# Performance work log

Hardware: AMD Instinct MI355X
Metric: run time of the kernel (lower is better)

## Reference

```python
import jax, jax.numpy as jnp
import numpy as np

NEG = -1e30  # finite stand-in for -inf (keeps grads nan-free)
BLANK = 0


def _ctc_nll(log_probs, targets, input_lengths, target_lengths):
    """Per-sample CTC negative log-likelihood.
    log_probs: (B,T,V) log-softmax outputs; targets: (B,S) int; lengths: (B,)."""
    B, T, V = log_probs.shape
    S = targets.shape[1]
    L = 2 * S + 1
    # extended label sequence: blank, y1, blank, y2, ..., blank -> (B, L)
    ext = jnp.full((B, L), BLANK, dtype=targets.dtype).at[:, 1::2].set(targets)
    # skip transition (l-2 -> l) allowed iff ext[l] != blank and ext[l] != ext[l-2]
    prev2 = jnp.pad(ext[:, :-2], ((0, 0), (2, 0)), constant_values=-1)
    skip = (ext != BLANK) & (ext != prev2)  # (B, L)

    def emit(lp_t):  # lp_t: (B,V) -> (B,L)
        return jnp.take_along_axis(lp_t, ext, axis=1)

    alpha0 = jnp.where(jnp.arange(L)[None, :] < 2, emit(log_probs[:, 0]), NEG)

    def step(alpha, lp_t):
        p1 = jnp.pad(alpha[:, :-1], ((0, 0), (1, 0)), constant_values=NEG)
        p2 = jnp.pad(alpha[:, :-2], ((0, 0), (2, 0)), constant_values=NEG)
        p2 = jnp.where(skip, p2, NEG)
        m = jnp.maximum(alpha, jnp.maximum(p1, p2))
        lse = m + jnp.log(jnp.exp(alpha - m) + jnp.exp(p1 - m) + jnp.exp(p2 - m))
        new = lse + emit(lp_t)
        return new, new

    # scan over time; collect alphas so we can read them at each sample's T_b-1
    _, alphas_rest = jax.lax.scan(step, alpha0, jnp.swapaxes(log_probs, 0, 1)[1:])
    alphas = jnp.concatenate([alpha0[None], alphas_rest], axis=0)  # (T,B,L)
    alphas = jnp.swapaxes(alphas, 0, 1)  # (B,T,L)
    alpha_T = jnp.take_along_axis(
        alphas, (input_lengths - 1)[:, None, None], axis=1)[:, 0]  # (B,L)

    end1 = jnp.take_along_axis(alpha_T, (2 * target_lengths)[:, None], axis=1)[:, 0]
    end2 = jnp.take_along_axis(alpha_T, (2 * target_lengths - 1)[:, None], axis=1)[:, 0]
    m = jnp.maximum(end1, end2)
    ll = m + jnp.log(jnp.exp(end1 - m) + jnp.exp(end2 - m))
    return -ll  # (B,)


def setup_inputs() -> dict:
    key = jax.random.key(0)
    k1, k2, k3, k4 = jax.random.split(key, 4)
    B, T, V, S = 32, 2000, 1024, 256
    log_probs = jax.nn.log_softmax(
        jax.random.normal(k1, (B, T, V), dtype=jnp.float32), axis=-1)
    targets = jax.random.randint(k2, (B, S), 1, V)  # exclude blank=0
    input_lengths = jax.random.randint(k3, (B,), 1500, T + 1)
    target_lengths = jax.random.randint(k4, (B,), 128, S + 1)
    return {"log_probs": log_probs, "targets": targets,
            "input_lengths": input_lengths, "target_lengths": target_lengths}


def reference(log_probs, targets, input_lengths, target_lengths):
    nll = _ctc_nll(log_probs, targets, input_lengths, target_lengths)
    # zero_infinity=True: drop infeasible samples
    nll = jnp.where(nll > 0.5 * (-NEG), 0.0, nll)
    # reduction='mean': divide each loss by its target length, then batch-mean
    return jnp.mean(nll / target_lengths.astype(nll.dtype))
```

## Files before the change

### kernel.cpp

```cpp
#include <hip/hip_runtime.h>
#include <stdint.h>


#define LN2F 0.69314718055994530942f
#define PD 16

__device__ __forceinline__ float shr1f(float x) {
  return __int_as_float(
      __builtin_amdgcn_update_dpp(0, __float_as_int(x), 0x138, 0xF, 0xF, true));
}
__device__ __forceinline__ int shr1i(int x) {
  return __builtin_amdgcn_update_dpp(0, x, 0x138, 0xF, 0xF, true);
}

__global__ __launch_bounds__(256) void k_gather_exp(
    const float* __restrict__ lp, const int* __restrict__ tgt,
    const int* __restrict__ ilen, float* __restrict__ El,
    float* __restrict__ Eb, int T, int V, int S) {
  const int b = blockIdx.y;
  const int t = blockIdx.x;
  if (t >= ilen[b]) return;
  const int tid = threadIdx.x;
  const int lab = tgt[b * S + tid];
  const float* row = lp + ((size_t)b * T + t) * V;
  El[((size_t)b * T + t) * S + tid] = __expf(row[lab]);
  if (tid == 0) Eb[(size_t)b * T + t] = __expf(row[0]);
}

__global__ __launch_bounds__(64) void k_ctc_alpha(
    const float* __restrict__ El, const float* __restrict__ Eb,
    const int* __restrict__ tgt, const int* __restrict__ ilen,
    const int* __restrict__ tlen, float* __restrict__ nll_out, int T, int S) {
  const int b = blockIdx.x;
  const int lane = threadIdx.x;
  const bool l0 = (lane == 0);

  const int Tb = ilen[b];
  const int U = tlen[b];

  const int4 tg = *(const int4*)(tgt + (size_t)b * S + 4 * lane);
  const int tprev = __shfl_up(tg.w, 1);
  const float sk0 = (l0 || tg.x != tprev) ? 1.0f : 0.0f;
  const float sk1 = (tg.y != tg.x) ? 1.0f : 0.0f;
  const float sk2 = (tg.z != tg.y) ? 1.0f : 0.0f;
  const float sk3 = (tg.w != tg.z) ? 1.0f : 0.0f;

  const float* Elb = El + (size_t)b * T * 256;
  const float* Ebb = Eb + (size_t)b * T;

  float a0 = l0 ? Ebb[0] : 0.0f;
  float aL0 = l0 ? Elb[0] : 0.0f;
  float aL1 = 0, aL2 = 0, aL3 = 0;
  float aB0 = 0, aB1 = 0, aB2 = 0, aB3 = 0;
  int o = 0;
  float s = 1.0f;

  auto stepf = [&](float4 el, float eb) {
    float pL = shr1f(aL3) * s;
    float pB = shr1f(aB3) * s;
    pL = l0 ? 0.0f : pL;
    pB = l0 ? a0 : pB;
    const float nB0 = (aB0 + aL0) * eb;
    const float nB1 = (aB1 + aL1) * eb;
    const float nB2 = (aB2 + aL2) * eb;
    const float nB3 = (aB3 + aL3) * eb;
    const float nL0 = (aL0 + fmaf(sk0, pL, pB)) * el.x;
    const float nL1 = (aL1 + fmaf(sk1, aL0, aB0)) * el.y;
    const float nL2 = (aL2 + fmaf(sk2, aL1, aB1)) * el.z;
    const float nL3 = (aL3 + fmaf(sk3, aL2, aB2)) * el.w;
    a0 *= eb;
    aL0 = nL0; aL1 = nL1; aL2 = nL2; aL3 = nL3;
    aB0 = nB0; aB1 = nB1; aB2 = nB2; aB3 = nB3;
  };
  auto renorm = [&]() {
    float m = fmaxf(fmaxf(fmaxf(aL0, aL1), fmaxf(aL2, aL3)),
                    fmaxf(fmaxf(aB0, aB1), fmaxf(aB2, aB3)));
    m = fmaxf(m, a0);
    const bool nz = (m > 0.0f);
    const int mk = nz ? (((__float_as_int(m) >> 23) & 0xff) - 126) : 0;
    const int ocand = o + mk;
    const int oleft = shr1i(ocand);
    o = (nz || l0) ? ocand : oleft;
    const float sc = nz ? __int_as_float((127 - mk) << 23) : 1.0f;
    aL0 *= sc; aL1 *= sc; aL2 *= sc; aL3 *= sc;
    aB0 *= sc; aB1 *= sc; aB2 *= sc; aB3 *= sc;
    a0 *= sc;
    int d = shr1i(o) - o;
    d = max(-126, min(126, d));
    s = __int_as_float((d + 127) << 23);
  };

  float4 pel[PD];
  float peb[PD];
  const int lo4 = 4 * lane;

#pragma unroll
  for (int j = 0; j < PD; ++j) {
    const int row = min(j + 1, Tb - 1);
    pel[j] = *(const float4*)(Elb + ((size_t)row << 8) + lo4);
    peb[j] = Ebb[row];
  }

  const int R = Tb - 1;
  const int nfull = R >> 4;
  const int rem = R & 15;

  for (int k = 0; k < nfull; ++k) {
    const int base = 1 + (k << 4);
#pragma unroll
    for (int j = 0; j < PD; ++j) {
      const float4 el = pel[j];
      const float eb = peb[j];
      const int row = min(base + PD + j, Tb - 1);
      pel[j] = *(const float4*)(Elb + ((size_t)row << 8) + lo4);
      peb[j] = Ebb[row];
      stepf(el, eb);
      if ((j & 3) == 2) renorm();
    }
  }
  {
#pragma unroll
    for (int j = 0; j < PD; ++j) {
      if (j < rem) {
        stepf(pel[j], peb[j]);
        if ((j & 3) == 2) renorm();
      }
    }
  }

  if (lane == ((U - 1) >> 2)) {
    const int j = (U - 1) & 3;
    float sv;
    if (j == 0)      sv = aL0 + aB0;
    else if (j == 1) sv = aL1 + aB1;
    else if (j == 2) sv = aL2 + aB2;
    else             sv = aL3 + aB3;
    float nll = -LN2F * (__log2f(sv) + (float)o);
    if (!(nll < 5e29f)) nll = 0.0f;
    nll_out[b] = nll / (float)U;
  }
}

__global__ __launch_bounds__(64) void k_reduce(const float* __restrict__ nll,
                                               float* __restrict__ out,
                                               int B) {
  float v = 0.0f;
  for (int i = threadIdx.x; i < B; i += 64) v += nll[i];
  for (int off = 32; off > 0; off >>= 1) v += __shfl_down(v, off);
  if (threadIdx.x == 0) out[0] = v / (float)B;
}

extern "C" void kernel_launch(void* const* d_in, const int* in_sizes, int n_in,
                              void* d_out, int out_size, void* d_ws,
                              size_t ws_size, hipStream_t stream) {
  const float* lp = (const float*)d_in[0];
  const int* tgt = (const int*)d_in[1];
  const int* ilen = (const int*)d_in[2];
  const int* tlen = (const int*)d_in[3];

  const int B = in_sizes[2];
  const int S = in_sizes[1] / B;
  const int V = 1024;
  const int T = (int)((size_t)in_sizes[0] / ((size_t)B * V));

  float* El = (float*)d_ws;
  float* Eb = El + (size_t)B * T * S;
  float* nw = Eb + (size_t)B * T;

  dim3 g1(T, B);
  k_gather_exp<<<g1, 256, 0, stream>>>(lp, tgt, ilen, El, Eb, T, V, S);
  k_ctc_alpha<<<B, 64, 0, stream>>>(El, Eb, tgt, ilen, tlen, nw, T, S);
  k_reduce<<<1, 64, 0, stream>>>(nw, (float*)d_out, B);
}
```

Baseline: 512.9 us.

## Double-buffer emission rows into LDS via async global_load_lds in CTC alpha kernel

Replaces the register-resident prefetch ring of float4 emission values with a two-buffer LDS staging scheme filled by asynchronous global-to-LDS copies, 16 time rows per chunk, gated by explicit vmcnt waits. The goal is to hide global memory latency on the serial recurrence without tying up many VGPRs in the prefetch ring. It also drops the lane-0 select on pL, which relies on the DPP shift feeding zero into lane 0, and moves the renormalisation step to a different position in each group of four. It adds LDS reads on every step plus hand-counted waitcnt values, with no barrier between the async LDS writes and the reads, so correctness depends on the hardware ordering those within the wavefront.

```diff
diff --git a/kernel.cpp b/kernel.cpp
--- a/kernel.cpp
+++ b/kernel.cpp
@@ -3,7 +3,16 @@
 
 
 #define LN2F 0.69314718055994530942f
-#define PD 16
+#define NR 16
+
+#define ASYNC_CP16(g, l)                                                     \
+  __builtin_amdgcn_global_load_lds(                                          \
+      (__attribute__((address_space(1))) void*)(g),                          \
+      (__attribute__((address_space(3))) void*)(l), 16, 0, 0)
+#define ASYNC_CP4(g, l)                                                      \
+  __builtin_amdgcn_global_load_lds(                                          \
+      (__attribute__((address_space(1))) void*)(g),                          \
+      (__attribute__((address_space(3))) void*)(l), 4, 0, 0)
 
 __device__ __forceinline__ float shr1f(float x) {
   return __int_as_float(
@@ -34,6 +43,8 @@
   const int b = blockIdx.x;
   const int lane = threadIdx.x;
   const bool l0 = (lane == 0);
+  __shared__ __align__(16) float elbuf[2][NR][256];
+  __shared__ __align__(16) float ebbuf[2][NR];
 
   const int Tb = ilen[b];
   const int U = tlen[b];
@@ -47,18 +58,27 @@
 
   const float* Elb = El + (size_t)b * T * 256;
   const float* Ebb = Eb + (size_t)b * T;
+  const int lo4 = 4 * lane;
 
-  float a0 = l0 ? Ebb[0] : 0.0f;
-  float aL0 = l0 ? Elb[0] : 0.0f;
-  float aL1 = 0, aL2 = 0, aL3 = 0;
+  float a0 = 0, aL0 = 0, aL1 = 0, aL2 = 0, aL3 = 0;
   float aB0 = 0, aB1 = 0, aB2 = 0, aB3 = 0;
   int o = 0;
   float s = 1.0f;
 
+  auto issue_chunk = [&](int c, int buf) {
+    const int base = c * NR;
+#pragma unroll
+    for (int r = 0; r < NR; ++r) {
+      const int row = min(base + r, Tb - 1);
+      ASYNC_CP16(Elb + ((size_t)row << 8) + lo4, &elbuf[buf][r][0]);
+    }
+    const int erow = min(base + (int)lane, Tb - 1);
+    if (lane < NR) ASYNC_CP4(Ebb + erow, &ebbuf[buf][0]);
+  };
+
   auto stepf = [&](float4 el, float eb) {
-    float pL = shr1f(aL3) * s;
+    const float pL = shr1f(aL3) * s;
     float pB = shr1f(aB3) * s;
-    pL = l0 ? 0.0f : pL;
     pB = l0 ? a0 : pB;
     const float nB0 = (aB0 + aL0) * eb;
     const float nB1 = (aB1 + aL1) * eb;
@@ -90,40 +110,42 @@
     s = __int_as_float((d + 127) << 23);
   };
 
-  float4 pel[PD];
-  float peb[PD];
-  const int lo4 = 4 * lane;
+  issue_chunk(0, 0);
+  const int nchunks = (Tb + NR - 1) / NR;
 
+  for (int c = 0; c < nchunks; ++c) {
+    const int buf = c & 1;
+    if (c + 1 < nchunks) {
+      issue_chunk(c + 1, buf ^ 1);
+      asm volatile("s_waitcnt vmcnt(17)" ::: "memory");
+    } else {
+      asm volatile("s_waitcnt vmcnt(0)" ::: "memory");
+    }
+    const int jend = min(NR, Tb - c * NR);
+    if (jend == NR) {
 #pragma unroll
-  for (int j = 0; j < PD; ++j) {
-    const int row = min(j + 1, Tb - 1);
-    pel[j] = *(const float4*)(Elb + ((size_t)row << 8) + lo4);
-    peb[j] = Ebb[row];
-  }
-
-  const int R = Tb - 1;
-  const int nfull = R >> 4;
-  const int rem = R & 15;
-
-  for (int k = 0; k < nfull; ++k) {
-    const int base = 1 + (k << 4);
-#pragma unroll
-    for (int j = 0; j < PD; ++j) {
-      const float4 el = pel[j];
-      const float eb = peb[j];
-      const int row = min(base + PD + j, Tb - 1);
-      pel[j] = *(const float4*)(Elb + ((size_t)row << 8) + lo4);
-      peb[j] = Ebb[row];
-      stepf(el, eb);
-      if ((j & 3) == 2) renorm();
-    }
-  }
-  {
-#pragma unroll
-    for (int j = 0; j < PD; ++j) {
-      if (j < rem) {
-        stepf(pel[j], peb[j]);
-        if ((j & 3) == 2) renorm();
+      for (int j = 0; j < NR; ++j) {
+        const float4 el = *(const float4*)&elbuf[buf][j][lo4];
+        const float eb = ebbuf[buf][j];
+        if (c == 0 && j == 0) {
+          a0 = l0 ? eb : 0.0f;
+          aL0 = l0 ? el.x : 0.0f;
+        } else {
+          stepf(el, eb);
+        }
+        if ((j & 3) == 3) renorm();
+      }
+    } else {
+      for (int j = 0; j < jend; ++j) {
+        const float4 el = *(const float4*)&elbuf[buf][j][lo4];
+        const float eb = ebbuf[buf][j];
+        if (c == 0 && j == 0) {
+          a0 = l0 ? eb : 0.0f;
+          aL0 = l0 ? el.x : 0.0f;
+        } else {
+          stepf(el, eb);
+        }
+        if ((j & 3) == 3) renorm();
       }
     }
   }
```

After: 536.1 us. 4.5% more time.
